# Optimization experiments

Hardware: AMD Instinct MI355X
Metric: run time of the kernel (lower is better)

## Reference

```python
import jax, jax.numpy as jnp
import numpy as np

N, E = 32768, 262144
IN_C, OUT_C = 128, 128
N_GRAPHS = 64


def setup_inputs() -> dict:
    key = jax.random.key(0)
    ks = jax.random.split(key, 8)
    x = jax.random.normal(ks[0], (N, IN_C), dtype=jnp.float32)
    edge_index = jax.random.randint(ks[1], (2, E), 0, N, dtype=jnp.int32)
    batch = jnp.sort(jax.random.randint(ks[2], (N,), 0, N_GRAPHS, dtype=jnp.int32))
    rand = jax.random.uniform(ks[3], (E,), dtype=jnp.float32)  # replaces random.random() draws
    lim_t = 1.0 / np.sqrt(IN_C)
    W_t = jax.random.uniform(ks[4], (IN_C, OUT_C), jnp.float32, -lim_t, lim_t)
    b_t = jax.random.uniform(ks[5], (OUT_C,), jnp.float32, -lim_t, lim_t)
    lim_s = 1.0 / np.sqrt(OUT_C)
    W_s = jax.random.uniform(ks[6], (OUT_C, 1), jnp.float32, -lim_s, lim_s)
    b_s = jax.random.uniform(ks[7], (1,), jnp.float32, -lim_s, lim_s)
    return dict(x=x, edge_index=edge_index, batch=batch, rand=rand,
                W_t=W_t, b_t=b_t, W_s=W_s, b_s=b_s)


def _greedy_match(scores, src, dst, rand, n):
    """Sequential greedy edge matching over score-sorted edges.
    Returns (order, cid_sorted, n_merged): cid_sorted[i] is the cluster id
    assigned to sorted edge i, or -1 if rejected/skipped."""
    scores = jax.lax.stop_gradient(scores)  # indices are non-differentiable (torch uses .item())
    rand = jax.lax.stop_gradient(rand)
    order = jnp.argsort(-scores)
    s_o, d_o = src[order], dst[order]
    acc = rand[order] <= scores[order]  # torch: skip edge if r > edge_score

    def step(carry, inp):
        avail, nxt = carry
        s, t, a = inp
        ok = a & avail[s] & avail[t]
        cid = jnp.where(ok, nxt, -1)
        avail = avail.at[s].set(avail[s] & ~ok)
        avail = avail.at[t].set(avail[t] & ~ok)
        return (avail, nxt + ok.astype(jnp.int32)), cid

    (_, n_merged), cid_sorted = jax.lax.scan(
        step, (jnp.ones((n,), bool), jnp.int32(0)), (s_o, d_o, acc))
    return order, cid_sorted, n_merged


def reference(x, edge_index, batch, rand, W_t, b_t, W_s, b_s):
    n = x.shape[0]
    src, dst = edge_index[0], edge_index[1]
    # merge_edge_sum + transform (eval mode, dropout p=0)
    x_merged = (x[src] + x[dst]) @ W_t + b_t          # [E, OUT_C]
    x_self = (x + x) @ W_t + b_t                      # [N, OUT_C] (self-edge merge)
    e = jax.nn.sigmoid((x_merged @ W_s).reshape(-1) + b_s[0])  # [E] edge scores

    order, cid_sorted, n_merged = _greedy_match(e, src, dst, rand, n)
    ok = cid_sorted >= 0                              # accepted sorted edges
    s_o, d_o = src[order], dst[order]

    # node -> cluster assignment (sentinel index n is dropped)
    cluster = jnp.full((n,), -1, jnp.int32)
    cluster = cluster.at[jnp.where(ok, s_o, n)].set(cid_sorted, mode='drop')
    cluster = cluster.at[jnp.where(ok, d_o, n)].set(cid_sorted, mode='drop')
    remaining = cluster < 0
    rem_rank = jnp.cumsum(remaining.astype(jnp.int32)) - 1  # ascending node order, like set iteration
    cluster = jnp.where(remaining, n_merged + rem_rank, cluster)
    num_clusters = n_merged + remaining.sum().astype(jnp.int32)

    # pooled features, padded to [n, OUT_C]; rows [0, num_clusters) are valid
    mcid = jnp.where(ok, cid_sorted, n)
    new_x = jnp.zeros((n, x_merged.shape[1]), x.dtype)
    new_x = new_x.at[mcid].set(x_merged[order], mode='drop')
    new_x = new_x.at[jnp.where(remaining, cluster, n)].set(x_self, mode='drop')

    # per-cluster edge score (1.0 for unmerged singleton nodes)
    new_edge_score = jnp.ones((n,), e.dtype).at[mcid].set(e[order], mode='drop')

    # new batch vector: new_batch[cluster[v]] = batch[v]
    new_batch = jnp.zeros((n,), batch.dtype).at[cluster].set(batch)

    # remapped edges + coalesce/remove_self_loops expressed as a validity mask
    new_ei = cluster[edge_index]                      # [2, E]
    key = new_ei[0].astype(jnp.int64) * n + new_ei[1].astype(jnp.int64)
    perm = jnp.argsort(key)
    ksorted = key[perm]
    first = jnp.concatenate([jnp.array([True]), ksorted[1:] != ksorted[:-1]])
    unique = jnp.zeros((key.shape[0],), bool).at[perm].set(first)
    edge_valid = unique & (new_ei[0] != new_ei[1])

    return new_x, cluster, new_batch, new_edge_score, num_clusters, new_ei, edge_valid, e
```

## Files before the change

### kernel.cpp

```cpp
#include <hip/hip_runtime.h>
#include <stdint.h>

typedef unsigned int u32;
typedef unsigned long long u64;

#define NN 32768
#define NE 262144
#define NC 128

#define O0 0u
#define O1 4194304u
#define O2 4227072u
#define O3 4259840u
#define O4 4292608u
#define O5 4292609u
#define O6 4816897u
#define O7 5079041u

#define HCAP (1u<<20)
#define NFULL 8
#define CNT0 8
#define MCAP 16384
#define SCAP 32768
#define SNB 32
#define MAXK 0xFFFFFFFFFFFFFFFFull
#define PREFLAG (1ull<<62)

__global__ void ep_prep(const float* Wt, const float* Ws, const float* bt, const float* bs,
                        double* u, double* c0, u32* counters) {
    int i = threadIdx.x;
    double s = 0.0;
    for (int j = 0; j < NC; j++) s += (double)Wt[i*NC+j] * (double)Ws[j];
    u[i] = s;
    if (i == 0) {
        double c = 0.0;
        for (int j = 0; j < NC; j++) c += (double)bt[j] * (double)Ws[j];
        *c0 = c + (double)bs[0];
    }
    if (i < 64) counters[i] = 0u;
}

__global__ void ep_init(u64* bt0, u64* bt1, u32* avail, int* cl) {
    int i = blockIdx.x*blockDim.x + threadIdx.x;
    if (i < NN) { bt0[i] = MAXK; bt1[i] = MAXK; cl[i] = -1; }
    if (i < NN/32) avail[i] = 0xFFFFFFFFu;
}

__global__ void ep_ynode(const float* x, const double* u, double* y) {
    int gid = blockIdx.x*blockDim.x + threadIdx.x;
    int v = gid >> 6, lane = threadIdx.x & 63;
    if (v >= NN) return;
    double t = (double)x[v*NC+lane]*u[lane] + (double)x[v*NC+lane+64]*u[lane+64];
    for (int off = 32; off; off >>= 1) t += __shfl_down(t, off, 64);
    if (lane == 0) y[v] = t;
}

__global__ void ep_escore(const int* src, const int* dst, const float* rnd, const double* y,
                          const double* c0, u64* fkey, u64* fdat, u32* counters, float* out) {
    int e = blockIdx.x*blockDim.x + threadIdx.x;
    if (e >= NE) return;
    int s = src[e], d = dst[e];
    double z = y[s] + y[d] + *c0;
    double sc = 1.0/(1.0 + exp(-z));
    out[O7 + e] = (float)sc;
    u64 b = (u64)__double_as_longlong(z);
    u64 ord = (b & 0x8000000000000000ull) ? ~b : (b | 0x8000000000000000ull);
    u64 P = ((~ord) & 0xFFFFFFFFFFFC0000ull) | (u64)(u32)e;
    if ((double)rnd[e] <= sc) {
        u32 p = atomicAdd(&counters[CNT0], 1u);
        fkey[p] = P;
        fdat[p] = ((u64)(u32)e << 30) | ((u64)(u32)s << 15) | (u64)(u32)d;
    }
}

__device__ __forceinline__ bool ep_bit(const u32* a, u32 v) { return (a[v>>5] >> (v&31)) & 1u; }

__global__ void ep_rA(const u64* fkey, const u64* fdat, const u32* cnt, u64* bt, const u32* avail) {
    u32 n = *cnt;
    for (u32 i = blockIdx.x*blockDim.x + threadIdx.x; i < n; i += 131072u) {
        u64 v = fdat[i];
        u32 s = (u32)((v>>15)&0x7FFF), d = (u32)(v&0x7FFF);
        if (ep_bit(avail, s) && ep_bit(avail, d)) {
            u64 P = fkey[i];
            atomicMin(&bt[s], P); atomicMin(&bt[d], P);
        }
    }
}

__global__ void ep_rB(const u64* fkey, const u64* fdat, const u32* cnt, u32* cntN,
                      u64* fkeyN, u64* fdatN, const u64* bt, u64* btN, u32* avail,
                      u64* mkey, u64* mpay, u32* counters) {
    u32 n = *cnt;
    for (u32 i = blockIdx.x*blockDim.x + threadIdx.x; i < n; i += 131072u) {
        u64 v = fdat[i];
        u32 s = (u32)((v>>15)&0x7FFF), d = (u32)(v&0x7FFF);
        if (!ep_bit(avail, s) || !ep_bit(avail, d)) continue;
        u64 P = fkey[i];
        if (bt[s] == P && bt[d] == P) {
            u32 slot = atomicAdd(&counters[2], 1u);
            mkey[slot] = P; mpay[slot] = v;
            atomicAnd(&avail[s>>5], ~(1u<<(s&31)));
            atomicAnd(&avail[d>>5], ~(1u<<(d&31)));
        } else {
            u32 p = atomicAdd(cntN, 1u);
            fkeyN[p] = P; fdatN[p] = v;
            btN[s] = MAXK; btN[d] = MAXK;
        }
    }
}

__global__ void ep_merge(const u64* mk, const u64* mp, const u64* fk, const u64* fd,
                         u32* counters, u64* ck, u64* cd2) {
    u32 i = blockIdx.x*blockDim.x + threadIdx.x;
    u32 nm0 = counters[2];
    u32 cr  = counters[CNT0+NFULL];
    if (i == 0) {
        u32 tot = nm0 + cr;
        counters[4] = tot > SCAP ? SCAP : tot;
    }
    u64 K = MAXK, D = 0;
    if (i < nm0) { K = mk[i]; D = mp[i] | PREFLAG; }
    else if (i < nm0 + cr && i < SCAP) { K = fk[i-nm0]; D = fd[i-nm0]; }
    ck[i] = K; cd2[i] = D;
}

__global__ void ms_hist(const u64* key, u32* hist, int shift) {
    __shared__ u32 h[256];
    int t = threadIdx.x;
    for (int i = t; i < 256; i += 64) h[i] = 0;
    __syncthreads();
    int base = blockIdx.x*1024 + t*16;
    for (int j = 0; j < 16; j++) {
        u32 dg = (u32)(key[base+j] >> shift) & 255u;
        atomicAdd(&h[dg], 1u);
    }
    __syncthreads();
    for (int i = t; i < 256; i += 64) hist[i*SNB + blockIdx.x] = h[i];
}

__global__ void ms_scan(u32* hist) {
    int t = threadIdx.x;
    int per = 256*SNB/64;
    int base = t*per;
    u32 s = 0;
    for (int j = 0; j < per; j++) s += hist[base+j];
    u32 x = s;
    for (int off = 1; off < 64; off <<= 1) { u32 yv = __shfl_up(x, off, 64); if (t >= off) x += yv; }
    u32 run = x - s;
    for (int j = 0; j < per; j++) { u32 tmp = hist[base+j]; hist[base+j] = run; run += tmp; }
}

__global__ void ms_scat(const u64* ki, const u64* pi, u64* ko, u64* po, const u32* hist, int shift) {
    __shared__ unsigned short m[256][64];
    int t = threadIdx.x;
    for (int i = t; i < 256*64/2; i += 64) ((u32*)m)[i] = 0u;
    __syncthreads();
    int base = blockIdx.x*1024 + t*16;
    u64 kr[16]; u32 dg[16];
    #pragma unroll
    for (int j = 0; j < 16; j++) {
        kr[j] = ki[base+j];
        dg[j] = (u32)(kr[j] >> shift) & 255u;
        m[dg[j]][t]++;
    }
    __syncthreads();
    for (int k = 0; k < 4; k++) {
        int d = t*4 + k;
        u32 run = 0;
        for (int tt = 0; tt < 64; tt++) { u32 tmp = m[d][tt]; m[d][tt] = (unsigned short)run; run += tmp; }
    }
    __syncthreads();
    #pragma unroll
    for (int j = 0; j < 16; j++) {
        u32 d = dg[j];
        u32 pos = hist[d*SNB + blockIdx.x] + m[d][t];
        m[d][t]++;
        ko[pos] = kr[j];
        po[pos] = pi[base+j];
    }
}

__global__ void __launch_bounds__(1024) ep_stail(const u64* sk, const u64* sd, const u32* availG,
                                                 u32* counters, u64* Mlist, int* cl) {
    __shared__ u32 avail[1024];
    __shared__ u32 claim[16384];
    __shared__ u32 wsum[16];
    __shared__ u32 cidBaseSh;
    int t = threadIdx.x;
    avail[t] = availG[t];
    for (int j = t; j < 16384; j += 1024) claim[j] = 0xFFFFFFFFu;
    if (t == 0) cidBaseSh = 0;
    __syncthreads();
    u32 cntT = counters[4];
    for (u32 base = 0; base < cntT; base += 1024) {
        u32 i = base + t;
        bool have = i < cntT;
        u64 P = 0, v = 0; u32 s = 0, d = 0; bool pre = false;
        if (have) {
            P = sk[i]; v = sd[i];
            pre = (v & PREFLAG) != 0;
            v &= ~PREFLAG;
            s = (u32)((v>>15)&0x7FFF); d = (u32)(v&0x7FFF);
        }
        (void)P;
        int st;
        if (!have) st = 1;
        else if (pre) st = 2;
        else st = (((avail[s>>5]>>(s&31))&1u) && ((avail[d>>5]>>(d&31))&1u)) ? 0 : 1;
        for (int it = 0; __syncthreads_count(st == 0) > 0 && it < 200; it++) {
            u32 hs = s & 16383u, hd = d & 16383u;
            bool wrote = false;
            if (st == 0) { atomicMin(&claim[hs], (u32)t); atomicMin(&claim[hd], (u32)t); wrote = true; }
            __syncthreads();
            if (st == 0 && claim[hs] == (u32)t && claim[hd] == (u32)t) {
                st = 2;
                atomicAnd(&avail[s>>5], ~(1u<<(s&31)));
                atomicAnd(&avail[d>>5], ~(1u<<(d&31)));
            }
            __syncthreads();
            if (wrote) { claim[hs] = 0xFFFFFFFFu; claim[hd] = 0xFFFFFFFFu; }
            if (st == 0) {
                if (!((avail[s>>5]>>(s&31))&1u) || !((avail[d>>5]>>(d&31))&1u)) st = 1;
            }
        }
        u32 m = (st == 2) ? 1u : 0u;
        u32 x = m;
        for (int off = 1; off < 64; off <<= 1) { u32 y = __shfl_up(x, off, 64); if ((t&63) >= off) x += y; }
        if ((t&63) == 63) wsum[t>>6] = x;
        __syncthreads();
        if (t < 16) {
            u32 ww = wsum[t];
            for (int off = 1; off < 16; off <<= 1) { u32 y = __shfl_up(ww, off, 16); if (t >= off) ww += y; }
            wsum[t] = ww;
        }
        __syncthreads();
        u32 excl = ((t>>6) ? wsum[(t>>6)-1] : 0u) + x - m;
        u32 cid = cidBaseSh + excl;
        if (m) {
            Mlist[cid] = v;
            cl[s] = (int)cid; cl[d] = (int)cid;
        }
        __syncthreads();
        if (t == 1023) cidBaseSh = cid + m;
        __syncthreads();
    }
    if (t == 0) counters[2] = cidBaseSh;
}

__global__ void ep_scanN(int* cl, u32* counters, float* out) {
    __shared__ u32 w[16];
    int t = threadIdx.x;
    int base = t*32;
    u32 s = 0;
    for (int j = 0; j < 32; j++) s += (cl[base+j] < 0) ? 1u : 0u;
    u32 x = s;
    for (int off = 1; off < 64; off <<= 1) { u32 y = __shfl_up(x, off, 64); if ((t&63) >= off) x += y; }
    if ((t&63) == 63) w[t>>6] = x;
    __syncthreads();
    if (t < 16) {
        u32 ww = w[t];
        for (int off = 1; off < 16; off <<= 1) { u32 y = __shfl_up(ww, off, 16); if (t >= off) ww += y; }
        w[t] = ww;
    }
    __syncthreads();
    u32 excl = ((t>>6) ? w[(t>>6)-1] : 0u) + x - s;
    u32 total = w[15];
    u32 nm = counters[2];
    if (t == 0) {
        counters[3] = nm + total;
        out[O4] = (float)(nm + total);
    }
    u32 run = nm + excl;
    for (int j = 0; j < 32; j++) { if (cl[base+j] < 0) cl[base+j] = (int)(run++); }
}

__global__ void ep_init_out(const u32* counters, float* out) {
    u32 i = blockIdx.x*blockDim.x + threadIdx.x;
    u32 nm = counters[2], ncl = counters[3];
    if (i < 4194304u) { if ((i>>7) >= ncl) out[O0 + i] = 0.0f; }
    if (i < 32768u) {
        if (i >= ncl) out[O2 + i] = 0.0f;
        if (i >= nm)  out[O3 + i] = 1.0f;
    }
}

__global__ void ep_out_nodes(const int* cl, const int* batch, const u32* counters, float* out) {
    int v = blockIdx.x*blockDim.x + threadIdx.x;
    if (v >= NN) return;
    int c = cl[v];
    out[O1 + v] = (float)c;
    if (c >= (int)counters[2]) out[O2 + c] = (float)batch[v];
}

__global__ void ep_out_matched(const u64* Mlist, const int* batch, const u32* counters, float* out) {
    u32 i = blockIdx.x*blockDim.x + threadIdx.x;
    if (i >= counters[2]) return;
    u64 v = Mlist[i];
    u32 e = (u32)(v>>30), s = (u32)((v>>15)&0x7FFF), d = (u32)(v&0x7FFF);
    u32 mx = s > d ? s : d;
    out[O2 + i] = (float)batch[mx];
    out[O3 + i] = out[O7 + e];
}

__global__ void ep_newx_m(const float* x, const float* Wt, const float* bt,
                          const u64* Mlist, const u32* counters, float* out) {
    __shared__ u64 ml[32];
    __shared__ float m[32][128];
    u32 nm = counters[2];
    u32 base = blockIdx.x * 32u;
    if (base >= nm) return;
    int t = threadIdx.x, lane = t & 63, wv = t >> 6;
    if (t < 32) { u32 r = base + (u32)t; ml[t] = (r < nm) ? Mlist[r] : 0ull; }
    __syncthreads();
    for (int i = t; i < 4096; i += 256) {
        int r = i >> 7, k = i & 127;
        u64 v = ml[r];
        u32 s = (u32)((v>>15)&0x7FFF), d = (u32)(v&0x7FFF);
        m[r][k] = x[s*NC+k] + x[d*NC+k];
    }
    __syncthreads();
    float a0[8], a1[8];
    #pragma unroll
    for (int r = 0; r < 8; r++) { a0[r] = bt[lane]; a1[r] = bt[lane+64]; }
    for (int k = 0; k < 128; k++) {
        float w0 = Wt[k*NC+lane], w1 = Wt[k*NC+lane+64];
        #pragma unroll
        for (int r = 0; r < 8; r++) { float mm = m[wv*8+r][k]; a0[r] += mm*w0; a1[r] += mm*w1; }
    }
    #pragma unroll
    for (int r = 0; r < 8; r++) {
        u32 row = base + (u32)(wv*8 + r);
        if (row < nm) {
            out[O0 + (size_t)row*NC + lane]      = a0[r];
            out[O0 + (size_t)row*NC + lane + 64] = a1[r];
        }
    }
}

__global__ void ep_newx_s(const float* x, const float* Wt, const float* bt,
                          const int* cl, const u32* counters, float* out) {
    __shared__ int rows[32];
    __shared__ float m[32][128];
    __shared__ int anyS;
    u32 nm = counters[2];
    u32 base = blockIdx.x * 32u;
    int t = threadIdx.x, lane = t & 63, wv = t >> 6;
    if (t == 0) anyS = 0;
    __syncthreads();
    if (t < 32) {
        rows[t] = cl[base + t];
        if (rows[t] >= (int)nm) atomicOr(&anyS, 1);
    }
    __syncthreads();
    if (!anyS) return;
    for (int i = t; i < 4096; i += 256) {
        int r = i >> 7, k = i & 127;
        m[r][k] = 2.0f * x[(base + r)*NC + k];
    }
    __syncthreads();
    float a0[8], a1[8];
    #pragma unroll
    for (int r = 0; r < 8; r++) { a0[r] = bt[lane]; a1[r] = bt[lane+64]; }
    for (int k = 0; k < 128; k++) {
        float w0 = Wt[k*NC+lane], w1 = Wt[k*NC+lane+64];
        #pragma unroll
        for (int r = 0; r < 8; r++) { float mm = m[wv*8+r][k]; a0[r] += mm*w0; a1[r] += mm*w1; }
    }
    #pragma unroll
    for (int r = 0; r < 8; r++) {
        int row = rows[wv*8 + r];
        if (row >= (int)nm) {
            out[O0 + (size_t)row*NC + lane]      = a0[r];
            out[O0 + (size_t)row*NC + lane + 64] = a1[r];
        }
    }
}

__global__ void ep_newei(const int* src, const int* dst, const int* cl,
                         u32* tkey, u32* tmin, u32* eslot, float* out) {
    int e = blockIdx.x*blockDim.x + threadIdx.x;
    if (e >= NE) return;
    u32 cs = (u32)cl[src[e]], cd = (u32)cl[dst[e]];
    out[O5 + e]      = (float)cs;
    out[O5 + NE + e] = (float)cd;
    u32 key = (cs << 15) | cd;
    u32 slot = ((key * 2654435761u) >> 12) & (HCAP-1);
    while (true) {
        u32 k = tkey[slot];
        if (k == key) break;
        if (k == 0xFFFFFFFFu) {
            u32 old = atomicCAS(&tkey[slot], 0xFFFFFFFFu, key);
            if (old == 0xFFFFFFFFu || old == key) break;
        }
        slot = (slot + 1) & (HCAP-1);
    }
    eslot[e] = slot;
    atomicMin(&tmin[slot], (u32)e);
}

__global__ void ep_valid(const int* src, const int* dst, const int* cl,
                         const u32* tmin, const u32* eslot, float* out) {
    int e = blockIdx.x*blockDim.x + threadIdx.x;
    if (e >= NE) return;
    u32 cs = (u32)cl[src[e]], cd = (u32)cl[dst[e]];
    bool valid = (tmin[eslot[e]] == (u32)e) && (cs != cd);
    out[O6 + e] = valid ? 1.0f : 0.0f;
}

extern "C" void kernel_launch(void* const* d_in, const int* in_sizes, int n_in,
                              void* d_out, int out_size, void* d_ws, size_t ws_size,
                              hipStream_t stream) {
    (void)in_sizes; (void)n_in; (void)out_size; (void)ws_size;
    const float* x    = (const float*)d_in[0];
    const int*   ei   = (const int*)d_in[1];
    const int*   src  = ei;
    const int*   dst  = ei + NE;
    const int*   batch= (const int*)d_in[2];
    const float* rnd  = (const float*)d_in[3];
    const float* Wt   = (const float*)d_in[4];
    const float* bt   = (const float*)d_in[5];
    const float* Ws   = (const float*)d_in[6];
    const float* bs   = (const float*)d_in[7];
    float* out = (float*)d_out;

    char* w = (char*)d_ws;
    double* u  = (double*)w;
    double* c0 = (double*)(w + 1024);
    u32* counters = (u32*)(w + 2048);
    size_t off = 4096;
    double* y   = (double*)(w + off); off += (size_t)NN*8;
    u64* fkeyA  = (u64*)(w + off); off += (size_t)NE*8;
    u64* fdatA  = (u64*)(w + off); off += (size_t)NE*8;
    u64* fkeyB  = (u64*)(w + off); off += (size_t)NE*8;
    u64* fdatB  = (u64*)(w + off); off += (size_t)NE*8;
    u64* mkeyA  = (u64*)(w + off); off += (size_t)MCAP*8;
    u64* mpayA  = (u64*)(w + off); off += (size_t)MCAP*8;
    u64* combK  = (u64*)(w + off); off += (size_t)SCAP*8;
    u64* combD  = (u64*)(w + off); off += (size_t)SCAP*8;
    u64* combK2 = (u64*)(w + off); off += (size_t)SCAP*8;
    u64* combD2 = (u64*)(w + off); off += (size_t)SCAP*8;
    u64* bt0    = (u64*)(w + off); off += (size_t)NN*8;
    u64* bt1    = (u64*)(w + off); off += (size_t)NN*8;
    u32* avail  = (u32*)(w + off); off += NN/8;
    int* cl     = (int*)(w + off); off += (size_t)NN*4;
    u64* Mlist  = (u64*)(w + off); off += (size_t)NN*8;
    u32* hist   = (u32*)(w + off); off += 256*SNB*4;
    u32* tkey   = (u32*)(w + off); off += (size_t)HCAP*4;
    u32* tmin   = (u32*)(w + off); off += (size_t)HCAP*4;
    u32* eslot  = (u32*)(w + off); off += (size_t)NE*4;

    ep_prep<<<1, 128, 0, stream>>>(Wt, Ws, bt, bs, u, c0, counters);
    ep_init<<<128, 256, 0, stream>>>(bt0, bt1, avail, cl);
    hipMemsetAsync(tkey, 0xFF, (size_t)HCAP*4, stream);
    hipMemsetAsync(tmin, 0xFF, (size_t)HCAP*4, stream);

    ep_ynode<<<8192, 256, 0, stream>>>(x, u, y);
    ep_escore<<<1024, 256, 0, stream>>>(src, dst, rnd, y, c0, fkeyA, fdatA, counters, out);

    u64 *fk = fkeyA, *fd = fdatA, *fk2 = fkeyB, *fd2 = fdatB;
    u64 *bc = bt0, *bn = bt1;
    for (u32 rd = 0; rd < NFULL; rd++) {
        ep_rA<<<512, 256, 0, stream>>>(fk, fd, &counters[CNT0+rd], bc, avail);
        ep_rB<<<512, 256, 0, stream>>>(fk, fd, &counters[CNT0+rd], &counters[CNT0+rd+1],
                                       fk2, fd2, bc, bn, avail, mkeyA, mpayA, counters);
        u64* tp;
        tp = fk; fk = fk2; fk2 = tp;
        tp = fd; fd = fd2; fd2 = tp;
        tp = bc; bc = bn; bn = tp;
    }

    ep_merge<<<SNB, 1024, 0, stream>>>(mkeyA, mpayA, fk, fd, counters, combK, combD);
    u64 *ki = combK, *pi = combD, *ko = combK2, *po = combD2;
    for (int p = 0; p < 6; p++) {
        int shift = 16 + p*8;
        ms_hist<<<SNB, 64, 0, stream>>>(ki, hist, shift);
        ms_scan<<<1, 64, 0, stream>>>(hist);
        ms_scat<<<SNB, 64, 0, stream>>>(ki, pi, ko, po, hist, shift);
        u64* tp;
        tp = ki; ki = ko; ko = tp;
        tp = pi; pi = po; po = tp;
    }
    ep_stail<<<1, 1024, 0, stream>>>(combK, combD, avail, counters, Mlist, cl);

    ep_scanN<<<1, 1024, 0, stream>>>(cl, counters, out);

    ep_init_out<<<16384, 256, 0, stream>>>(counters, out);
    ep_out_nodes<<<128, 256, 0, stream>>>(cl, batch, counters, out);
    ep_out_matched<<<64, 256, 0, stream>>>(Mlist, batch, counters, out);

    ep_newx_m<<<512, 256, 0, stream>>>(x, Wt, bt, Mlist, counters, out);
    ep_newx_s<<<1024, 256, 0, stream>>>(x, Wt, bt, cl, counters, out);

    ep_newei<<<1024, 256, 0, stream>>>(src, dst, cl, tkey, tmin, eslot, out);
    ep_valid<<<1024, 256, 0, stream>>>(src, dst, cl, tmin, eslot, out);
}
```

Before: 695.4 us.

## Compact tail candidates and parallelize match emission; shrink dedup hash table

```diff
diff --git a/kernel.cpp b/kernel.cpp
--- a/kernel.cpp
+++ b/kernel.cpp
@@ -17,7 +17,7 @@
 #define O6 4816897u
 #define O7 5079041u
 
-#define HCAP (1u<<20)
+#define HCAP (1u<<19)
 #define NFULL 8
 #define CNT0 8
 #define MCAP 16384
@@ -180,34 +180,71 @@
     }
 }
 
-__global__ void __launch_bounds__(1024) ep_stail(const u64* sk, const u64* sd, const u32* availG,
-                                                 u32* counters, u64* Mlist, int* cl) {
+__global__ void ep_csum(const u64* sd, const u32* counters, u32* mflag, u32* csums) {
+    u32 i = blockIdx.x*1024 + threadIdx.x;
+    u32 cnt = counters[4];
+    u64 v = sd[i];
+    bool pre = (i < cnt) && ((v & PREFLAG) != 0);
+    bool cand = (i < cnt) && !pre;
+    mflag[i] = pre ? 1u : 0u;
+    int c = __syncthreads_count(cand ? 1 : 0);
+    if (threadIdx.x == 0) csums[blockIdx.x] = (u32)c;
+}
+
+__global__ void ep_cscan(u32* csums, u32* counters, int which) {
+    int t = threadIdx.x;
+    u32 v = (t < SNB) ? csums[t] : 0u;
+    u32 x = v;
+    for (int off = 1; off < 64; off <<= 1) { u32 y = __shfl_up(x, off, 64); if (t >= off) x += y; }
+    if (t < SNB) csums[t] = x - v;
+    if (t == SNB-1) counters[which] = x;
+}
+
+__global__ void ep_cemit(const u64* sd, const u32* counters, const u32* csums, u32* candIdx) {
+    __shared__ u32 w[16];
+    int t = threadIdx.x;
+    u32 i = blockIdx.x*1024 + t;
+    u32 cnt = counters[4];
+    u64 v = sd[i];
+    bool pre = (i < cnt) && ((v & PREFLAG) != 0);
+    u32 c = ((i < cnt) && !pre) ? 1u : 0u;
+    u32 x = c;
+    for (int off = 1; off < 64; off <<= 1) { u32 y = __shfl_up(x, off, 64); if ((t&63) >= off) x += y; }
+    if ((t&63) == 63) w[t>>6] = x;
+    __syncthreads();
+    if (t < 16) {
+        u32 ww = w[t];
+        for (int off = 1; off < 16; off <<= 1) { u32 y = __shfl_up(ww, off, 16); if (t >= off) ww += y; }
+        w[t] = ww;
+    }
+    __syncthreads();
+    u32 excl = ((t>>6) ? w[(t>>6)-1] : 0u) + x - c;
+    if (c) candIdx[csums[blockIdx.x] + excl] = i;
+}
+
+__global__ void __launch_bounds__(1024) ep_walk(const u64* sd, const u32* candIdx,
+                                                const u32* counters, const u32* availG,
+                                                u32* mflag) {
     __shared__ u32 avail[1024];
     __shared__ u32 claim[16384];
-    __shared__ u32 wsum[16];
-    __shared__ u32 cidBaseSh;
     int t = threadIdx.x;
     avail[t] = availG[t];
     for (int j = t; j < 16384; j += 1024) claim[j] = 0xFFFFFFFFu;
-    if (t == 0) cidBaseSh = 0;
-    __syncthreads();
-    u32 cntT = counters[4];
-    for (u32 base = 0; base < cntT; base += 1024) {
-        u32 i = base + t;
-        bool have = i < cntT;
-        u64 P = 0, v = 0; u32 s = 0, d = 0; bool pre = false;
+    __syncthreads();
+    u32 ncand = counters[5];
+    for (u32 base = 0; base < ncand; base += 1024) {
+        u32 j = base + t;
+        bool have = j < ncand;
+        u32 i = 0, s = 0, d = 0;
         if (have) {
-            P = sk[i]; v = sd[i];
-            pre = (v & PREFLAG) != 0;
-            v &= ~PREFLAG;
+            i = candIdx[j];
+            u64 v = sd[i];
             s = (u32)((v>>15)&0x7FFF); d = (u32)(v&0x7FFF);
         }
-        (void)P;
         int st;
         if (!have) st = 1;
-        else if (pre) st = 2;
         else st = (((avail[s>>5]>>(s&31))&1u) && ((avail[d>>5]>>(d&31))&1u)) ? 0 : 1;
-        for (int it = 0; __syncthreads_count(st == 0) > 0 && it < 200; it++) {
+        for (int it = 0; __syncthreads_count(st == 0) > 0 && it < 300; it++) {
             u32 hs = s & 16383u, hd = d & 16383u;
             bool wrote = false;
             if (st == 0) { atomicMin(&claim[hs], (u32)t); atomicMin(&claim[hd], (u32)t); wrote = true; }
@@ -223,31 +260,47 @@
                 if (!((avail[s>>5]>>(s&31))&1u) || !((avail[d>>5]>>(d&31))&1u)) st = 1;
             }
         }
-        u32 m = (st == 2) ? 1u : 0u;
-        u32 x = m;
-        for (int off = 1; off < 64; off <<= 1) { u32 y = __shfl_up(x, off, 64); if ((t&63) >= off) x += y; }
-        if ((t&63) == 63) wsum[t>>6] = x;
+        if (st == 2) mflag[i] = 1u;
         __syncthreads();
-        if (t < 16) {
-            u32 ww = wsum[t];
-            for (int off = 1; off < 16; off <<= 1) { u32 y = __shfl_up(ww, off, 16); if (t >= off) ww += y; }
-            wsum[t] = ww;
-        }
-        __syncthreads();
-        u32 excl = ((t>>6) ? wsum[(t>>6)-1] : 0u) + x - m;
-        u32 cid = cidBaseSh + excl;
-        if (m) {
-            Mlist[cid] = v;
-            cl[s] = (int)cid; cl[d] = (int)cid;
-        }
-        __syncthreads();
-        if (t == 1023) cidBaseSh = cid + m;
-        __syncthreads();
-    }
-    if (t == 0) counters[2] = cidBaseSh;
-}
-
-__global__ void ep_scanN(int* cl, u32* counters, float* out) {
+    }
+}
+
+__global__ void ep_msum(const u32* mflag, u32* msums) {
+    u32 i = blockIdx.x*1024 + threadIdx.x;
+    int c = __syncthreads_count(mflag[i] != 0 ? 1 : 0);
+    if (threadIdx.x == 0) msums[blockIdx.x] = (u32)c;
+}
+
+__global__ void ep_memit(const u64* sd, const u32* mflag, const u32* msums,
+                         const int* batch, u64* Mlist, int* cl, float* out) {
+    __shared__ u32 w[16];
+    int t = threadIdx.x;
+    u32 i = blockIdx.x*1024 + t;
+    u32 m = mflag[i];
+    u32 x = m;
+    for (int off = 1; off < 64; off <<= 1) { u32 y = __shfl_up(x, off, 64); if ((t&63) >= off) x += y; }
+    if ((t&63) == 63) w[t>>6] = x;
+    __syncthreads();
+    if (t < 16) {
+        u32 ww = w[t];
+        for (int off = 1; off < 16; off <<= 1) { u32 y = __shfl_up(ww, off, 16); if (t >= off) ww += y; }
+        w[t] = ww;
+    }
+    __syncthreads();
+    u32 excl = ((t>>6) ? w[(t>>6)-1] : 0u) + x - m;
+    if (m) {
+        u32 cid = msums[blockIdx.x] + excl;
+        u64 v = sd[i] & ~PREFLAG;
+        u32 e = (u32)(v>>30), s = (u32)((v>>15)&0x7FFF), d = (u32)(v&0x7FFF);
+        Mlist[cid] = v;
+        cl[s] = (int)cid; cl[d] = (int)cid;
+        u32 mx = s > d ? s : d;
+        out[O2 + cid] = (float)batch[mx];
+        out[O3 + cid] = out[O7 + e];
+    }
+}
+
+__global__ void ep_scanN(int* cl, u32* counters, u32* slist, float* out) {
     __shared__ u32 w[16];
     int t = threadIdx.x;
     int base = t*32;
@@ -268,10 +321,16 @@
     u32 nm = counters[2];
     if (t == 0) {
         counters[3] = nm + total;
+        counters[6] = total;
         out[O4] = (float)(nm + total);
     }
     u32 run = nm + excl;
-    for (int j = 0; j < 32; j++) { if (cl[base+j] < 0) cl[base+j] = (int)(run++); }
+    for (int j = 0; j < 32; j++) {
+        if (cl[base+j] < 0) {
+            slist[run - nm] = (u32)(base + j);
+            cl[base+j] = (int)(run++);
+        }
+    }
 }
 
 __global__ void ep_init_out(const u32* counters, float* out) {
@@ -290,16 +349,6 @@
     int c = cl[v];
     out[O1 + v] = (float)c;
     if (c >= (int)counters[2]) out[O2 + c] = (float)batch[v];
-}
-
-__global__ void ep_out_matched(const u64* Mlist, const int* batch, const u32* counters, float* out) {
-    u32 i = blockIdx.x*blockDim.x + threadIdx.x;
-    if (i >= counters[2]) return;
-    u64 v = Mlist[i];
-    u32 e = (u32)(v>>30), s = (u32)((v>>15)&0x7FFF), d = (u32)(v&0x7FFF);
-    u32 mx = s > d ? s : d;
-    out[O2 + i] = (float)batch[mx];
-    out[O3 + i] = out[O7 + e];
 }
 
 __global__ void ep_newx_m(const float* x, const float* Wt, const float* bt,
@@ -338,24 +387,19 @@
 }
 
 __global__ void ep_newx_s(const float* x, const float* Wt, const float* bt,
-                          const int* cl, const u32* counters, float* out) {
-    __shared__ int rows[32];
+                          const u32* slist, const u32* counters, float* out) {
+    __shared__ u32 nodes[32];
     __shared__ float m[32][128];
-    __shared__ int anyS;
+    u32 sc = counters[6];
     u32 nm = counters[2];
     u32 base = blockIdx.x * 32u;
+    if (base >= sc) return;
     int t = threadIdx.x, lane = t & 63, wv = t >> 6;
-    if (t == 0) anyS = 0;
-    __syncthreads();
-    if (t < 32) {
-        rows[t] = cl[base + t];
-        if (rows[t] >= (int)nm) atomicOr(&anyS, 1);
-    }
-    __syncthreads();
-    if (!anyS) return;
+    if (t < 32) { u32 p = base + (u32)t; nodes[t] = (p < sc) ? slist[p] : slist[sc-1]; }
+    __syncthreads();
     for (int i = t; i < 4096; i += 256) {
         int r = i >> 7, k = i & 127;
-        m[r][k] = 2.0f * x[(base + r)*NC + k];
+        m[r][k] = 2.0f * x[nodes[r]*NC + k];
     }
     __syncthreads();
     float a0[8], a1[8];
@@ -368,8 +412,9 @@
     }
     #pragma unroll
     for (int r = 0; r < 8; r++) {
-        int row = rows[wv*8 + r];
-        if (row >= (int)nm) {
+        u32 p = base + (u32)(wv*8 + r);
+        if (p < sc) {
+            u32 row = nm + p;
             out[O0 + (size_t)row*NC + lane]      = a0[r];
             out[O0 + (size_t)row*NC + lane + 64] = a1[r];
         }
@@ -384,7 +429,7 @@
     out[O5 + e]      = (float)cs;
     out[O5 + NE + e] = (float)cd;
     u32 key = (cs << 15) | cd;
-    u32 slot = ((key * 2654435761u) >> 12) & (HCAP-1);
+    u32 slot = ((key * 2654435761u) >> 11) & (HCAP-1);
     while (true) {
         u32 k = tkey[slot];
         if (k == key) break;
@@ -445,6 +490,11 @@
     int* cl     = (int*)(w + off); off += (size_t)NN*4;
     u64* Mlist  = (u64*)(w + off); off += (size_t)NN*8;
     u32* hist   = (u32*)(w + off); off += 256*SNB*4;
+    u32* mflag  = (u32*)(w + off); off += (size_t)SCAP*4;
+    u32* candIdx= (u32*)(w + off); off += (size_t)SCAP*4;
+    u32* csums  = (u32*)(w + off); off += 64*4;
+    u32* msums  = (u32*)(w + off); off += 64*4;
+    u32* slist  = (u32*)(w + off); off += (size_t)NN*4;
     u32* tkey   = (u32*)(w + off); off += (size_t)HCAP*4;
     u32* tmin   = (u32*)(w + off); off += (size_t)HCAP*4;
     u32* eslot  = (u32*)(w + off); off += (size_t)NE*4;
@@ -480,16 +530,22 @@
         tp = ki; ki = ko; ko = tp;
         tp = pi; pi = po; po = tp;
     }
-    ep_stail<<<1, 1024, 0, stream>>>(combK, combD, avail, counters, Mlist, cl);
-
-    ep_scanN<<<1, 1024, 0, stream>>>(cl, counters, out);
+
+    ep_csum<<<SNB, 1024, 0, stream>>>(combD, counters, mflag, csums);
+    ep_cscan<<<1, 64, 0, stream>>>(csums, counters, 5);
+    ep_cemit<<<SNB, 1024, 0, stream>>>(combD, counters, csums, candIdx);
+    ep_walk<<<1, 1024, 0, stream>>>(combD, candIdx, counters, avail, mflag);
+    ep_msum<<<SNB, 1024, 0, stream>>>(mflag, msums);
+    ep_cscan<<<1, 64, 0, stream>>>(msums, counters, 2);
+    ep_memit<<<SNB, 1024, 0, stream>>>(combD, mflag, msums, batch, Mlist, cl, out);
+
+    ep_scanN<<<1, 1024, 0, stream>>>(cl, counters, slist, out);
 
     ep_init_out<<<16384, 256, 0, stream>>>(counters, out);
     ep_out_nodes<<<128, 256, 0, stream>>>(cl, batch, counters, out);
-    ep_out_matched<<<64, 256, 0, stream>>>(Mlist, batch, counters, out);
 
     ep_newx_m<<<512, 256, 0, stream>>>(x, Wt, bt, Mlist, counters, out);
-    ep_newx_s<<<1024, 256, 0, stream>>>(x, Wt, bt, cl, counters, out);
+    ep_newx_s<<<1024, 256, 0, stream>>>(x, Wt, bt, slist, counters, out);
 
     ep_newei<<<1024, 256, 0, stream>>>(src, dst, cl, tkey, tmin, eslot, out);
     ep_valid<<<1024, 256, 0, stream>>>(src, dst, cl, tmin, eslot, out);
```

Measured after the change: 665.5 us. 1.04x faster.
